# Performance work log

Hardware: AMD Instinct MI355X
Metric: run time of the kernel (lower is better)

## Reference

```python
import jax, jax.numpy as jnp
import numpy as np
from jax import lax

B, N_SITES, FEAT, BOND, OUT = 2048, 128, 64, 32, 256
CORE_SCALE = 0.02  # keeps the 128-step matrix product finite


def setup_inputs() -> dict:
    key = jax.random.key(0)
    ks = jax.random.split(key, 6)
    return {
        "x": jax.random.normal(ks[0], (B, N_SITES, FEAT), dtype=jnp.float32),
        "cores": jax.random.normal(ks[1], (N_SITES, BOND, FEAT, BOND), dtype=jnp.float32) * CORE_SCALE,
        "start": jax.random.normal(ks[2], (1, BOND), dtype=jnp.float32),
        "end": jax.random.normal(ks[3], (BOND, 1), dtype=jnp.float32),
        "fc_w": jax.random.normal(ks[4], (OUT, 1), dtype=jnp.float32),
        "fc_b": jax.random.normal(ks[5], (OUT,), dtype=jnp.float32),
    }


def reference(x, cores, start, end, fc_w, fc_b):
    # x: [B, N, F]; cores: [N, D, F, D]; start: [1, D]; end: [D, 1]
    b = x.shape[0]
    res0 = jnp.broadcast_to(start, (b, start.shape[1]))  # [B, D]

    def step(res, site):
        xi, core = site  # xi: [B, F], core: [D, F, D]
        m = jnp.einsum('bf,dfr->bdr', xi, core)  # per-site transfer matrix [B, D, D]
        return jnp.einsum('bd,bdr->br', res, m), None

    res, _ = lax.scan(step, res0, (jnp.swapaxes(x, 0, 1), cores))
    val = res @ end  # [B, 1]
    return val @ fc_w.T + fc_b  # [B, OUT]
```

## Files before the change

### kernel.cpp

```cpp
#include <hip/hip_runtime.h>


#define NSITES 128
#define FEATD  64
#define BOND   32
#define OUTD   256
#define BT     32
#define SEGLEN 32
#define NSEG   (NSITES / SEGLEN)
#define NBT    (2048 / BT)

#define RSTRIDE 48
#define BSTRIDE 1552

typedef __attribute__((ext_vector_type(4))) float float4v;

__device__ __forceinline__ unsigned pk4_fp8(float a, float b, float c, float d) {
    int v = __builtin_amdgcn_cvt_pk_fp8_f32(a, b, 0, false);
    v = __builtin_amdgcn_cvt_pk_fp8_f32(c, d, v, true);
    return (unsigned)v;
}

__global__ __launch_bounds__(256)
void prep_cores8(const float* __restrict__ cores, unsigned char* __restrict__ core8) {
    __shared__ float tile[FEATD][BOND + 4];
    const int nd = blockIdx.x;
    const int t  = threadIdx.x;
    const float* src = cores + (size_t)nd * (FEATD * BOND);
    {
        int base = t * 8;
        int f = base >> 5, r0 = base & 31;
        float4 v0 = *(const float4*)(src + base);
        float4 v1 = *(const float4*)(src + base + 4);
        tile[f][r0 + 0] = v0.x; tile[f][r0 + 1] = v0.y;
        tile[f][r0 + 2] = v0.z; tile[f][r0 + 3] = v0.w;
        tile[f][r0 + 4] = v1.x; tile[f][r0 + 5] = v1.y;
        tile[f][r0 + 6] = v1.z; tile[f][r0 + 7] = v1.w;
    }
    __syncthreads();
    const int r = t >> 3, f0 = (t & 7) * 8;
    const float s = 16.0f;
    unsigned lo = pk4_fp8(tile[f0 + 0][r] * s, tile[f0 + 1][r] * s,
                          tile[f0 + 2][r] * s, tile[f0 + 3][r] * s);
    unsigned hi = pk4_fp8(tile[f0 + 4][r] * s, tile[f0 + 5][r] * s,
                          tile[f0 + 6][r] * s, tile[f0 + 7][r] * s);
    uint2 w; w.x = lo; w.y = hi;
    *(uint2*)(core8 + ((size_t)nd * BOND + r) * FEATD + f0) = w;
}

__global__ __launch_bounds__(1024, 4)
void mps_seg(const float* __restrict__ x, const unsigned char* __restrict__ core8,
             unsigned char* __restrict__ Pout) {
    __shared__ __align__(16) unsigned char MS[BT * BSTRIDE];
    __shared__ __align__(16) unsigned char XS[BT * 72];

    const int t    = threadIdx.x;
    const int wave = t >> 6;
    const int lane = t & 63;
    const int cl   = lane & 15;
    const int q    = lane >> 4;
    const int cb   = wave & 7;
    const int bh   = wave >> 3;
    const int b0   = blockIdx.x * BT;
    const int seg  = blockIdx.y;

    int pw[2][2][2];
#pragma unroll
    for (int bi = 0; bi < 2; ++bi)
#pragma unroll
        for (int I = 0; I < 2; ++I)
#pragma unroll
            for (int J = 0; J < 2; ++J) {
                int v = 0;
                int g = cl - 4 * q;
                if (I == J && g >= 0 && g < 4) v = 0x58 << (g * 8);
                pw[bi][I][J] = v;
            }

    const int hi32  = (lane & 32) ? 1 : 0;
    const int addr0 = (cl + ((lane & 16) << 1)) * 4;
    const int addr1 = addr0 + 64;

    const int xb = t >> 5, xf = (t & 31) * 2;
    const unsigned afoff = (unsigned)((cb * 8 * 16 + cl) * FEATD + q * 8);

    {
        float2 x0 = *(const float2*)(x + ((size_t)(b0 + xb) * NSITES + seg * SEGLEN) * FEATD + xf);
        int v = __builtin_amdgcn_cvt_pk_fp8_f32(x0.x, x0.y, 0, false);
        *(unsigned short*)&XS[xb * 72 + xf] = (unsigned short)(v & 0xffff);
    }
    long af[16];
    {
        const unsigned char* p0 = core8 + (size_t)(seg * SEGLEN) * (1024 * FEATD) + afoff;
#pragma unroll
        for (int i = 0; i < 8; ++i) {
            af[i * 2 + 0] = *(const long*)(p0 + i * (16 * FEATD));
            af[i * 2 + 1] = *(const long*)(p0 + i * (16 * FEATD) + 32);
        }
    }

    for (int k = 0; k < SEGLEN; ++k) {
        const int n = seg * SEGLEN + k;
        __syncthreads();

        long bx0 = *(const long*)&XS[(bh * 16 + cl) * 72 + q * 8];
        long bx1 = *(const long*)&XS[(bh * 16 + cl) * 72 + 32 + q * 8];
        float4v acc[8];
#pragma unroll
        for (int i = 0; i < 8; ++i) {
            float4v z = {0.f, 0.f, 0.f, 0.f};
            z = __builtin_amdgcn_mfma_f32_16x16x32_fp8_fp8(af[i * 2 + 0], bx0, z, 0, 0, 0);
            acc[i] = __builtin_amdgcn_mfma_f32_16x16x32_fp8_fp8(af[i * 2 + 1], bx1, z, 0, 0, 0);
        }
#pragma unroll
        for (int p = 0; p < 2; ++p)
#pragma unroll
            for (int g = 0; g < 4; ++g) {
                unsigned w = pk4_fp8(acc[p][g], acc[p + 2][g], acc[p + 4][g], acc[p + 6][g]);
                *(unsigned*)&MS[(bh * 16 + cl) * BSTRIDE + (16 * p + 4 * q + g) * RSTRIDE + cb * 4] = w;
            }

        __syncthreads();

        float2 xn;
        if (k + 1 < SEGLEN) {
            xn = *(const float2*)(x + ((size_t)(b0 + xb) * NSITES + n + 1) * FEATD + xf);
            const unsigned char* p1 = core8 + (size_t)(n + 1) * (1024 * FEATD) + afoff;
#pragma unroll
            for (int i = 0; i < 8; ++i) {
                af[i * 2 + 0] = *(const long*)(p1 + i * (16 * FEATD));
                af[i * 2 + 1] = *(const long*)(p1 + i * (16 * FEATD) + 32);
            }
        }

#pragma unroll
        for (int bi = 0; bi < 2; ++bi) {
            const int bb = wave * 2 + bi;
            long pa0 = *(const long*)&MS[bb * BSTRIDE + (0 * 16 + cl) * RSTRIDE + q * 8];
            long pa1 = *(const long*)&MS[bb * BSTRIDE + (1 * 16 + cl) * RSTRIDE + q * 8];
            long pbv[2];
#pragma unroll
            for (int h = 0; h < 2; ++h) {
                int l0a = __builtin_amdgcn_ds_bpermute(addr0, pw[bi][0][h]);
                int l0b = __builtin_amdgcn_ds_bpermute(addr0, pw[bi][1][h]);
                int l1a = __builtin_amdgcn_ds_bpermute(addr1, pw[bi][0][h]);
                int l1b = __builtin_amdgcn_ds_bpermute(addr1, pw[bi][1][h]);
                int d0 = hi32 ? l0b : l0a;
                int d1 = hi32 ? l1b : l1a;
                pbv[h] = ((long)(unsigned)d0) | (((long)d1) << 32);
            }
            float4v pc[2][2];
#pragma unroll
            for (int I = 0; I < 2; ++I)
#pragma unroll
                for (int J = 0; J < 2; ++J) {
                    float4v z = {0.f, 0.f, 0.f, 0.f};
                    pc[I][J] = __builtin_amdgcn_mfma_f32_16x16x32_fp8_fp8(
                        I ? pa1 : pa0, pbv[J], z, 0, 0, 0);
                }
#pragma unroll
            for (int I = 0; I < 2; ++I)
#pragma unroll
                for (int J = 0; J < 2; ++J)
                    pw[bi][I][J] = (int)pk4_fp8(pc[I][J][0] * 0.0625f, pc[I][J][1] * 0.0625f,
                                                pc[I][J][2] * 0.0625f, pc[I][J][3] * 0.0625f);
        }

        if (k + 1 < SEGLEN) {
            int v = __builtin_amdgcn_cvt_pk_fp8_f32(xn.x, xn.y, 0, false);
            *(unsigned short*)&XS[xb * 72 + xf] = (unsigned short)(v & 0xffff);
        }
    }

    __syncthreads();
#pragma unroll
    for (int bi = 0; bi < 2; ++bi) {
        const int bb = wave * 2 + bi;
#pragma unroll
        for (int I = 0; I < 2; ++I)
#pragma unroll
            for (int J = 0; J < 2; ++J)
                *(unsigned*)&MS[bb * 1024 + (J * 16 + cl) * 32 + I * 16 + q * 4] =
                    (unsigned)pw[bi][I][J];
    }
    __syncthreads();
    {
        int b = t >> 5, chunk = t & 31;
        const uint4* p = (const uint4*)&MS[b * 1024 + chunk * 32];
        uint4 v0 = p[0];
        uint4 v1 = p[1];
        uint4* g = (uint4*)(Pout + (((size_t)seg * 2048 + b0 + b) * 1024 + chunk * 32));
        g[0] = v0;
        g[1] = v1;
    }
}

__global__ __launch_bounds__(512)
void combine(const unsigned char* __restrict__ Pout, const float* __restrict__ startv,
             const float* __restrict__ endv, const float* __restrict__ fc_w,
             const float* __restrict__ fc_b, float* __restrict__ out) {
    const int t    = threadIdx.x;
    const int wave = t >> 6;
    const int lane = t & 63;
    const int r    = lane >> 1;
    const int dh   = lane & 1;
    const int b    = blockIdx.x * 8 + wave;

    float res = startv[r];
    const unsigned char* base = Pout + (size_t)b * 1024 + dh * 512 + r;

    unsigned char by[16];
#pragma unroll
    for (int di = 0; di < 16; ++di) by[di] = base[di * 32];

    for (int s = 0; s < NSEG; ++s) {
        unsigned char by2[16];
        if (s + 1 < NSEG) {
            const unsigned char* nb = base + (size_t)(s + 1) * 2048 * 1024;
#pragma unroll
            for (int di = 0; di < 16; ++di) by2[di] = nb[di * 32];
        }
        float acc = 0.f;
#pragma unroll
        for (int di = 0; di < 16; ++di) {
            float rv = __shfl(res, dh * 32 + di * 2, 64);
            acc += rv * __builtin_amdgcn_cvt_f32_fp8((int)by[di], 0);
        }
        float tot = acc + __shfl_xor(acc, 1, 64);
        res = tot * 0.0625f;
        if (s + 1 < NSEG) {
#pragma unroll
            for (int di = 0; di < 16; ++di) by[di] = by2[di];
        }
    }

    float v = dh ? 0.f : res * endv[r];
#pragma unroll
    for (int off = 1; off < 64; off <<= 1) v += __shfl_xor(v, off, 64);

    const int j = lane * 4;
    float4 w4  = *(const float4*)(fc_w + j);
    float4 bb4 = *(const float4*)(fc_b + j);
    float4 o;
    o.x = v * w4.x + bb4.x;
    o.y = v * w4.y + bb4.y;
    o.z = v * w4.z + bb4.z;
    o.w = v * w4.w + bb4.w;
    *(float4*)(out + (size_t)b * OUTD + j) = o;
}

extern "C" void kernel_launch(void* const* d_in, const int* in_sizes, int n_in,
                              void* d_out, int out_size, void* d_ws, size_t ws_size,
                              hipStream_t stream) {
    const float* x      = (const float*)d_in[0];
    const float* cores  = (const float*)d_in[1];
    const float* startv = (const float*)d_in[2];
    const float* endv   = (const float*)d_in[3];
    const float* fc_w   = (const float*)d_in[4];
    const float* fc_b   = (const float*)d_in[5];
    float* out = (float*)d_out;

    unsigned char* core8 = (unsigned char*)d_ws;
    unsigned char* Pout  = core8 + (size_t)NSITES * 1024 * FEATD;

    prep_cores8<<<NSITES * BOND, 256, 0, stream>>>(cores, core8);
    mps_seg<<<dim3(NBT, NSEG), 1024, 0, stream>>>(x, core8, Pout);
    combine<<<2048 / 8, 512, 0, stream>>>(Pout, startv, endv, fc_w, fc_b, out);
}
```

Measured before the change: 268.7 us.

## Use 32x32x16 FP8 MFMA for per-batch chain product with 16-row batch tiles

The batch tile shrinks from 32 to 16 rows and the block from 1024 to 512 threads. Each wave now owns one 128-column slice of the transfer matrices for all 16 batch rows. The per-batch 32x32 running product is computed with two 32x32x16 FP8 MFMAs instead of four 16x16x32 ones. That cuts the bpermute shuffles from eight to four per batch, and the matrix shared-memory layout is transposed to suit it. The final result is written straight from registers to global memory, dropping a shared-memory staging pass and two barriers. In exchange, core fragments are reloaded by twice as many blocks, and there is less batch reuse per core load.

```diff
diff --git a/kernel.cpp b/kernel.cpp
--- a/kernel.cpp
+++ b/kernel.cpp
@@ -5,20 +5,24 @@
 #define FEATD  64
 #define BOND   32
 #define OUTD   256
-#define BT     32
+#define BT     16
 #define SEGLEN 32
 #define NSEG   (NSITES / SEGLEN)
 #define NBT    (2048 / BT)
 
-#define RSTRIDE 48
-#define BSTRIDE 1552
-
-typedef __attribute__((ext_vector_type(4))) float float4v;
+#define MS_RS  648
+#define MS_BS  40
+
+typedef __attribute__((ext_vector_type(4)))  float float4v;
+typedef __attribute__((ext_vector_type(16))) float float16v;
 
 __device__ __forceinline__ unsigned pk4_fp8(float a, float b, float c, float d) {
     int v = __builtin_amdgcn_cvt_pk_fp8_f32(a, b, 0, false);
     v = __builtin_amdgcn_cvt_pk_fp8_f32(c, d, v, true);
     return (unsigned)v;
+}
+__device__ __forceinline__ long mklong(int lo, int hi) {
+    return ((long)(unsigned)lo) | (((long)hi) << 32);
 }
 
 __global__ __launch_bounds__(256)
@@ -48,10 +52,10 @@
     *(uint2*)(core8 + ((size_t)nd * BOND + r) * FEATD + f0) = w;
 }
 
-__global__ __launch_bounds__(1024, 4)
+__global__ __launch_bounds__(512, 4)
 void mps_seg(const float* __restrict__ x, const unsigned char* __restrict__ core8,
              unsigned char* __restrict__ Pout) {
-    __shared__ __align__(16) unsigned char MS[BT * BSTRIDE];
+    __shared__ __align__(16) unsigned char MS[BOND * MS_RS];
     __shared__ __align__(16) unsigned char XS[BT * 72];
 
     const int t    = threadIdx.x;
@@ -59,36 +63,30 @@
     const int lane = t & 63;
     const int cl   = lane & 15;
     const int q    = lane >> 4;
-    const int cb   = wave & 7;
-    const int bh   = wave >> 3;
+    const int l    = lane & 31;
+    const int h    = lane >> 5;
     const int b0   = blockIdx.x * BT;
     const int seg  = blockIdx.y;
 
-    int pw[2][2][2];
-#pragma unroll
-    for (int bi = 0; bi < 2; ++bi)
-#pragma unroll
-        for (int I = 0; I < 2; ++I)
-#pragma unroll
-            for (int J = 0; J < 2; ++J) {
-                int v = 0;
-                int g = cl - 4 * q;
-                if (I == J && g >= 0 && g < 4) v = 0x58 << (g * 8);
-                pw[bi][I][J] = v;
-            }
-
-    const int hi32  = (lane & 32) ? 1 : 0;
-    const int addr0 = (cl + ((lane & 16) << 1)) * 4;
-    const int addr1 = addr0 + 64;
+    int pq[2][4];
+    {
+        int g0 = l >> 3;
+        int hm = ((l >> 2) & 1) == h;
+#pragma unroll
+        for (int bi = 0; bi < 2; ++bi)
+#pragma unroll
+            for (int g = 0; g < 4; ++g)
+                pq[bi][g] = (g == g0 && hm) ? (0x58 << ((l & 3) * 8)) : 0;
+    }
+    const int paddr = (lane ^ 32) << 2;
 
     const int xb = t >> 5, xf = (t & 31) * 2;
-    const unsigned afoff = (unsigned)((cb * 8 * 16 + cl) * FEATD + q * 8);
-
     {
         float2 x0 = *(const float2*)(x + ((size_t)(b0 + xb) * NSITES + seg * SEGLEN) * FEATD + xf);
         int v = __builtin_amdgcn_cvt_pk_fp8_f32(x0.x, x0.y, 0, false);
         *(unsigned short*)&XS[xb * 72 + xf] = (unsigned short)(v & 0xffff);
     }
+    const unsigned afoff = (unsigned)((wave * 128 + cl) * FEATD + q * 8);
     long af[16];
     {
         const unsigned char* p0 = core8 + (size_t)(seg * SEGLEN) * (1024 * FEATD) + afoff;
@@ -103,8 +101,8 @@
         const int n = seg * SEGLEN + k;
         __syncthreads();
 
-        long bx0 = *(const long*)&XS[(bh * 16 + cl) * 72 + q * 8];
-        long bx1 = *(const long*)&XS[(bh * 16 + cl) * 72 + 32 + q * 8];
+        long bx0 = *(const long*)&XS[cl * 72 + q * 8];
+        long bx1 = *(const long*)&XS[cl * 72 + 32 + q * 8];
         float4v acc[8];
 #pragma unroll
         for (int i = 0; i < 8; ++i) {
@@ -117,7 +115,7 @@
 #pragma unroll
             for (int g = 0; g < 4; ++g) {
                 unsigned w = pk4_fp8(acc[p][g], acc[p + 2][g], acc[p + 4][g], acc[p + 6][g]);
-                *(unsigned*)&MS[(bh * 16 + cl) * BSTRIDE + (16 * p + 4 * q + g) * RSTRIDE + cb * 4] = w;
+                *(unsigned*)&MS[(16 * p + 4 * q + g) * MS_RS + cl * MS_BS + wave * 4] = w;
             }
 
         __syncthreads();
@@ -136,34 +134,23 @@
 #pragma unroll
         for (int bi = 0; bi < 2; ++bi) {
             const int bb = wave * 2 + bi;
-            long pa0 = *(const long*)&MS[bb * BSTRIDE + (0 * 16 + cl) * RSTRIDE + q * 8];
-            long pa1 = *(const long*)&MS[bb * BSTRIDE + (1 * 16 + cl) * RSTRIDE + q * 8];
-            long pbv[2];
-#pragma unroll
-            for (int h = 0; h < 2; ++h) {
-                int l0a = __builtin_amdgcn_ds_bpermute(addr0, pw[bi][0][h]);
-                int l0b = __builtin_amdgcn_ds_bpermute(addr0, pw[bi][1][h]);
-                int l1a = __builtin_amdgcn_ds_bpermute(addr1, pw[bi][0][h]);
-                int l1b = __builtin_amdgcn_ds_bpermute(addr1, pw[bi][1][h]);
-                int d0 = hi32 ? l0b : l0a;
-                int d1 = hi32 ? l1b : l1a;
-                pbv[h] = ((long)(unsigned)d0) | (((long)d1) << 32);
-            }
-            float4v pc[2][2];
-#pragma unroll
-            for (int I = 0; I < 2; ++I)
-#pragma unroll
-                for (int J = 0; J < 2; ++J) {
-                    float4v z = {0.f, 0.f, 0.f, 0.f};
-                    pc[I][J] = __builtin_amdgcn_mfma_f32_16x16x32_fp8_fp8(
-                        I ? pa1 : pa0, pbv[J], z, 0, 0, 0);
-                }
-#pragma unroll
-            for (int I = 0; I < 2; ++I)
-#pragma unroll
-                for (int J = 0; J < 2; ++J)
-                    pw[bi][I][J] = (int)pk4_fp8(pc[I][J][0] * 0.0625f, pc[I][J][1] * 0.0625f,
-                                                pc[I][J][2] * 0.0625f, pc[I][J][3] * 0.0625f);
+            long a0 = *(const long*)&MS[l * MS_RS + bb * MS_BS + 8 * h];
+            long a1 = *(const long*)&MS[l * MS_RS + bb * MS_BS + 16 + 8 * h];
+            int x0 = __builtin_amdgcn_ds_bpermute(paddr, pq[bi][0]);
+            int x1 = __builtin_amdgcn_ds_bpermute(paddr, pq[bi][1]);
+            int x2 = __builtin_amdgcn_ds_bpermute(paddr, pq[bi][2]);
+            int x3 = __builtin_amdgcn_ds_bpermute(paddr, pq[bi][3]);
+            long bf0 = h ? mklong(x1, pq[bi][1]) : mklong(pq[bi][0], x0);
+            long bf1 = h ? mklong(x3, pq[bi][3]) : mklong(pq[bi][2], x2);
+            float16v pc;
+#pragma unroll
+            for (int i = 0; i < 16; ++i) pc[i] = 0.f;
+            pc = __builtin_amdgcn_mfma_f32_32x32x16_fp8_fp8(a0, bf0, pc, 0, 0, 0);
+            pc = __builtin_amdgcn_mfma_f32_32x32x16_fp8_fp8(a1, bf1, pc, 0, 0, 0);
+#pragma unroll
+            for (int g = 0; g < 4; ++g)
+                pq[bi][g] = (int)pk4_fp8(pc[4 * g + 0] * 0.0625f, pc[4 * g + 1] * 0.0625f,
+                                         pc[4 * g + 2] * 0.0625f, pc[4 * g + 3] * 0.0625f);
         }
 
         if (k + 1 < SEGLEN) {
@@ -172,26 +159,13 @@
         }
     }
 
-    __syncthreads();
 #pragma unroll
     for (int bi = 0; bi < 2; ++bi) {
         const int bb = wave * 2 + bi;
-#pragma unroll
-        for (int I = 0; I < 2; ++I)
-#pragma unroll
-            for (int J = 0; J < 2; ++J)
-                *(unsigned*)&MS[bb * 1024 + (J * 16 + cl) * 32 + I * 16 + q * 4] =
-                    (unsigned)pw[bi][I][J];
-    }
-    __syncthreads();
-    {
-        int b = t >> 5, chunk = t & 31;
-        const uint4* p = (const uint4*)&MS[b * 1024 + chunk * 32];
-        uint4 v0 = p[0];
-        uint4 v1 = p[1];
-        uint4* g = (uint4*)(Pout + (((size_t)seg * 2048 + b0 + b) * 1024 + chunk * 32));
-        g[0] = v0;
-        g[1] = v1;
+        unsigned char* gp = Pout + (((size_t)seg * 2048 + b0 + bb) * 1024);
+#pragma unroll
+        for (int g = 0; g < 4; ++g)
+            *(unsigned*)(gp + l * 32 + 8 * g + 4 * h) = (unsigned)pq[bi][g];
     }
 }
 
@@ -264,6 +238,6 @@
     unsigned char* Pout  = core8 + (size_t)NSITES * 1024 * FEATD;
 
     prep_cores8<<<NSITES * BOND, 256, 0, stream>>>(cores, core8);
-    mps_seg<<<dim3(NBT, NSEG), 1024, 0, stream>>>(x, core8, Pout);
+    mps_seg<<<dim3(NBT, NSEG), 512, 0, stream>>>(x, core8, Pout);
     combine<<<2048 / 8, 512, 0, stream>>>(Pout, startv, endv, fc_w, fc_b, out);
 }
```

New measurement: 253.0 us. 5.8% less time.
